# Performance work log

Measured on AMD Instinct MI355X. Metric: run time of the kernel, lower is better.

The kernel has to match this reference:

```python
import jax, jax.numpy as jnp
import numpy as np

N, C, T, H, W = 8, 512, 8, 32, 32
CI = 256          # inter_channels = in_channels // 2
CA = 128          # audio feature dim (hard-coded nn.Linear(128, in_channels))
BN_EPS = 1e-5
LN_EPS = 1e-5


def setup_inputs() -> dict:
    key = jax.random.key(0)
    ks = jax.random.split(key, 8)
    s = 0.02
    f32 = jnp.float32
    return {
        "x": jax.random.normal(ks[0], (N, C, T, H, W), f32),
        "audio": jax.random.normal(ks[1], (N, T, CA), f32),
        "align_W": jax.random.normal(ks[2], (C, CA), f32) * s,
        "align_b": jnp.zeros((C,), f32),
        "Wg": jax.random.normal(ks[3], (CI, C), f32) * s,
        "bg": jnp.zeros((CI,), f32),
        "Wth": jax.random.normal(ks[4], (CI, C), f32) * s,
        "bth": jnp.zeros((CI,), f32),
        "Wph": jax.random.normal(ks[5], (CI, C), f32) * s,
        "bph": jnp.zeros((CI,), f32),
        "Wz": jax.random.normal(ks[6], (C, CI), f32) * s,
        "bz": jnp.zeros((C,), f32),
        "bn_gamma": jnp.ones((C,), f32),
        "bn_beta": jnp.zeros((C,), f32),
        "ln_gamma": jnp.ones((C,), f32),
        "ln_beta": jnp.zeros((C,), f32),
    }


def reference(x, audio, align_W, align_b, Wg, bg, Wth, bth, Wph, bph,
              Wz, bz, bn_gamma, bn_beta, ln_gamma, ln_beta):
    n, c, t, h, w = x.shape
    thw = t * h * w

    # align_channel: Linear(128, C) + ReLU on audio (N,T,128) -> (N,T,C)
    audio_temp = jax.nn.relu(jnp.einsum('ntk,ck->ntc', audio, align_W) + align_b)
    a = audio_temp.transpose(0, 2, 1)  # (N,C,T); broadcast over (H,W) kept implicit

    # 1x1x1 conv projections (== per-token linear maps)
    g_x = (jnp.einsum('oc,ncthw->nthwo', Wg, x) + bg).reshape(n, thw, CI)      # (N,THW,CI)
    theta_x = (jnp.einsum('oc,ncthw->nthwo', Wth, x) + bth).reshape(n, thw, CI)
    phi_a = jnp.einsum('oc,nct->not', Wph, a) + bph[None, :, None]             # (N,CI,T)

    # mode='dot' attention. phi(audio) is constant over (h,w): the full score
    # matrix f[n,s,(t,h,w)] equals f_small[n,s,t], so f@g factorizes exactly.
    f_small = jnp.einsum('nsi,nit->nst', theta_x, phi_a)   # (N,THW,T)
    f_div = f_small / thw                                  # f / N_tokens
    G = g_x.reshape(n, t, h * w, CI).sum(axis=2)           # (N,T,CI): sum of g over repeated hw
    y = jnp.einsum('nst,nto->nso', f_div, G)               # (N,THW,CI)
    y = y.transpose(0, 2, 1).reshape(n, CI, t, h, w)

    # W_z: 1x1x1 conv (CI->C) + BatchNorm3d (training-mode batch stats)
    W_y = jnp.einsum('oc,ncthw->nothw', Wz, y) + bz[None, :, None, None, None]
    mu = W_y.mean(axis=(0, 2, 3, 4), keepdims=True)
    var = W_y.var(axis=(0, 2, 3, 4), keepdims=True)
    W_y = (W_y - mu) * jax.lax.rsqrt(var + BN_EPS)
    W_y = W_y * bn_gamma[None, :, None, None, None] + bn_beta[None, :, None, None, None]

    # residual blend + LayerNorm over channel dim
    z = 0.5 * W_y + 0.5 * x
    zp = z.transpose(0, 2, 3, 4, 1)  # (N,T,H,W,C)
    mu2 = zp.mean(axis=-1, keepdims=True)
    var2 = zp.var(axis=-1, keepdims=True)
    zp = (zp - mu2) * jax.lax.rsqrt(var2 + LN_EPS) * ln_gamma + ln_beta
    z = zp.transpose(0, 4, 1, 2, 3)  # (N,C,T,H,W)
    return z, audio_temp
```

## Files before the change

kernel.cpp:

```cpp
#include <hip/hip_runtime.h>


__global__ __launch_bounds__(256) void k_small1(
    const float* __restrict__ audio, const float* __restrict__ alignW, const float* __restrict__ alignB,
    const float* __restrict__ Wph, const float* __restrict__ bph,
    const float* __restrict__ Wth, const float* __restrict__ bth,
    float* __restrict__ outA, float* __restrict__ constT, float* __restrict__ M)
{
    int b = blockIdx.x; int n = b >> 3; int t = b & 7; int tid = threadIdx.x;
    __shared__ float al[128];
    __shared__ float atl[512];
    __shared__ float phil[256];
    __shared__ float red[256];
    if (tid < 128) al[tid] = audio[(n * 8 + t) * 128 + tid];
    __syncthreads();
    for (int c = tid; c < 512; c += 256) {
        float a0 = alignB[c], a1 = 0.f, a2 = 0.f, a3 = 0.f;
        const float* Wr = alignW + c * 128;
        #pragma unroll 4
        for (int k = 0; k < 128; k += 4) {
            a0 += al[k] * Wr[k];         a1 += al[k + 1] * Wr[k + 1];
            a2 += al[k + 2] * Wr[k + 2]; a3 += al[k + 3] * Wr[k + 3];
        }
        float acc = fmaxf((a0 + a1) + (a2 + a3), 0.f);
        atl[c] = acc;
        outA[(n * 8 + t) * 512 + c] = acc;
    }
    __syncthreads();
    {
        int i = tid;
        float a0 = bph[i], a1 = 0.f, a2 = 0.f, a3 = 0.f;
        const float* Wr = Wph + i * 512;
        #pragma unroll 4
        for (int c = 0; c < 512; c += 4) {
            a0 += Wr[c] * atl[c];         a1 += Wr[c + 1] * atl[c + 1];
            a2 += Wr[c + 2] * atl[c + 2]; a3 += Wr[c + 3] * atl[c + 3];
        }
        float acc = (a0 + a1) + (a2 + a3);
        phil[i] = acc;
        red[i] = acc * bth[i];
    }
    __syncthreads();
    for (int sr = 128; sr > 0; sr >>= 1) {
        if (tid < sr) red[tid] += red[tid + sr];
        __syncthreads();
    }
    if (tid == 0) constT[n * 8 + t] = red[0];
    for (int c = tid; c < 512; c += 256) {
        float a0 = 0.f, a1 = 0.f, a2 = 0.f, a3 = 0.f;
        #pragma unroll 4
        for (int i = 0; i < 256; i += 4) {
            a0 += Wth[i * 512 + c] * phil[i];
            a1 += Wth[(i + 1) * 512 + c] * phil[i + 1];
            a2 += Wth[(i + 2) * 512 + c] * phil[i + 2];
            a3 += Wth[(i + 3) * 512 + c] * phil[i + 3];
        }
        M[n * 4096 + c * 8 + t] = (a0 + a1) + (a2 + a3);
    }
}

__global__ __launch_bounds__(256) void k_xsum(const float* __restrict__ x, float* __restrict__ xs)
{
    int row = blockIdx.x * 4 + (threadIdx.x >> 6);
    int lane = threadIdx.x & 63;
    const float4* p = reinterpret_cast<const float4*>(x + (size_t)row * 1024);
    float s = 0.f;
    #pragma unroll
    for (int k = 0; k < 4; ++k) {
        float4 v = p[lane + 64 * k];
        s += v.x + v.y + v.z + v.w;
    }
    for (int off = 32; off > 0; off >>= 1) s += __shfl_down(s, off);
    if (lane == 0) xs[row] = s;
}

__global__ __launch_bounds__(512, 4) void k_fsmall(
    const float* __restrict__ x, const float* __restrict__ M,
    const float* __restrict__ constT, float* __restrict__ fs,
    float* __restrict__ Part)
{
    int b = blockIdx.x; int n = b >> 6; int s0 = (b & 63) << 7;
    int tid = threadIdx.x; int lane = tid & 63; int wv = tid >> 6;
    __shared__ float Ml[512][8];
    {
        const float4* src = reinterpret_cast<const float4*>(M + n * 4096);
        float4* dst = reinterpret_cast<float4*>(&Ml[0][0]);
        for (int i = tid; i < 1024; i += 512) dst[i] = src[i];
    }
    __syncthreads();
    const float* xb = x + (size_t)n * 4194304 + s0 + lane * 2;
    float2 p2[8];
    #pragma unroll
    for (int k = 0; k < 8; ++k) p2[k] = make_float2(0.f, 0.f);
    #pragma unroll 8
    for (int j = 0; j < 64; ++j) {
        int c = wv * 64 + j;
        float2 xv = *reinterpret_cast<const float2*>(xb + (size_t)c * 8192);
        float4 m0 = *reinterpret_cast<const float4*>(&Ml[c][0]);
        float4 m1 = *reinterpret_cast<const float4*>(&Ml[c][4]);
        p2[0].x = fmaf(xv.x, m0.x, p2[0].x); p2[0].y = fmaf(xv.y, m0.x, p2[0].y);
        p2[1].x = fmaf(xv.x, m0.y, p2[1].x); p2[1].y = fmaf(xv.y, m0.y, p2[1].y);
        p2[2].x = fmaf(xv.x, m0.z, p2[2].x); p2[2].y = fmaf(xv.y, m0.z, p2[2].y);
        p2[3].x = fmaf(xv.x, m0.w, p2[3].x); p2[3].y = fmaf(xv.y, m0.w, p2[3].y);
        p2[4].x = fmaf(xv.x, m1.x, p2[4].x); p2[4].y = fmaf(xv.y, m1.x, p2[4].y);
        p2[5].x = fmaf(xv.x, m1.y, p2[5].x); p2[5].y = fmaf(xv.y, m1.y, p2[5].y);
        p2[6].x = fmaf(xv.x, m1.z, p2[6].x); p2[6].y = fmaf(xv.y, m1.z, p2[6].y);
        p2[7].x = fmaf(xv.x, m1.w, p2[7].x); p2[7].y = fmaf(xv.y, m1.w, p2[7].y);
    }
    __shared__ float ldsT[8][8][130];
    #pragma unroll
    for (int k = 0; k < 8; ++k)
        *reinterpret_cast<float2*>(&ldsT[wv][k][lane * 2]) = p2[k];
    __syncthreads();
    __shared__ float partm[2][44];
    if (tid < 128) {
        int tok = tid; int wq = tid >> 6;
        const float* ct = constT + n * 8;
        float q[8];
        #pragma unroll
        for (int k = 0; k < 8; ++k) {
            float v = ct[k];
            #pragma unroll
            for (int g = 0; g < 8; ++g) v += ldsT[g][k][tok];
            q[k] = v;
        }
        float4* op = reinterpret_cast<float4*>(fs + ((size_t)n * 8192 + s0 + tok) * 8);
        op[0] = make_float4(q[0], q[1], q[2], q[3]);
        op[1] = make_float4(q[4], q[5], q[6], q[7]);
        float mom[44];
        {
            int idx = 8;
            for (int t1 = 0; t1 < 8; ++t1) {
                mom[t1] = q[t1];
                for (int t2 = t1; t2 < 8; ++t2) { mom[idx] = q[t1] * q[t2]; ++idx; }
            }
        }
        for (int k = 0; k < 44; ++k)
            for (int off = 32; off > 0; off >>= 1) mom[k] += __shfl_down(mom[k], off);
        if ((tid & 63) == 0)
            for (int k = 0; k < 44; ++k) partm[wq][k] = mom[k];
    }
    __syncthreads();
    if (tid < 44) Part[b * 44 + tid] = partm[0][tid] + partm[1][tid];
}

__global__ __launch_bounds__(256) void k_small2(
    const float* __restrict__ xs, const float* __restrict__ Wg, const float* __restrict__ bg,
    const float* __restrict__ Wz, float* __restrict__ GW)
{
    int b = blockIdx.x; int n = b >> 3; int t = b & 7; int tid = threadIdx.x;
    __shared__ float xsl[512];
    __shared__ float gl[256];
    for (int c = tid; c < 512; c += 256) xsl[c] = xs[(n * 512 + c) * 8 + t];
    __syncthreads();
    {
        int o = tid;
        float a0 = 1024.f * bg[o], a1 = 0.f, a2 = 0.f, a3 = 0.f;
        const float* Wr = Wg + o * 512;
        #pragma unroll 4
        for (int c = 0; c < 512; c += 4) {
            a0 += Wr[c] * xsl[c];         a1 += Wr[c + 1] * xsl[c + 1];
            a2 += Wr[c + 2] * xsl[c + 2]; a3 += Wr[c + 3] * xsl[c + 3];
        }
        gl[o] = (a0 + a1) + (a2 + a3);
    }
    __syncthreads();
    for (int c = tid; c < 512; c += 256) {
        float a0 = 0.f, a1 = 0.f, a2 = 0.f, a3 = 0.f;
        const float* Wr = Wz + c * 256;
        #pragma unroll 4
        for (int o = 0; o < 256; o += 4) {
            a0 += Wr[o] * gl[o];         a1 += Wr[o + 1] * gl[o + 1];
            a2 += Wr[o + 2] * gl[o + 2]; a3 += Wr[o + 3] * gl[o + 3];
        }
        GW[(n * 8 + t) * 512 + c] = (a0 + a1) + (a2 + a3);
    }
}

__global__ __launch_bounds__(512) void k_bn(
    const float* __restrict__ Part, const float* __restrict__ GW,
    const float* __restrict__ bz, const float* __restrict__ bng, const float* __restrict__ bnb,
    const float* __restrict__ lng, const float* __restrict__ lnb,
    float* __restrict__ pack0, float* __restrict__ gw2)
{
    int n0 = blockIdx.x; int c = threadIdx.x;
    __shared__ float Fl[64];
    __shared__ float S2l[512];
    if (c < 352) {
        int n = c / 44, k = c % 44;
        float v = 0.f;
        for (int i = 0; i < 64; ++i) v += Part[(n * 64 + i) * 44 + k];
        if (k < 8) Fl[n * 8 + k] = v;
        else {
            int kk = k - 8; int t1 = 0;
            while (kk >= 8 - t1) { kk -= 8 - t1; ++t1; }
            int t2 = t1 + kk;
            S2l[n * 64 + t1 * 8 + t2] = v;
            S2l[n * 64 + t2 * 8 + t1] = v;
        }
    }
    __syncthreads();
    const float r = 1.f / 8192.f;
    float meanu = 0.f, e2 = 0.f;
    for (int n = 0; n < 8; ++n) {
        float g[8];
        for (int t = 0; t < 8; ++t) g[t] = GW[(n * 8 + t) * 512 + c];
        for (int t = 0; t < 8; ++t) meanu += Fl[n * 8 + t] * g[t];
        for (int t1 = 0; t1 < 8; ++t1)
            for (int t2 = 0; t2 < 8; ++t2) e2 += S2l[n * 64 + t1 * 8 + t2] * g[t1] * g[t2];
    }
    const float invCnt = 1.f / 65536.f;
    meanu *= r * invCnt;
    e2 *= r * r * invCnt;
    float var = fmaxf(e2 - meanu * meanu, 0.f);
    float bzv = bz[c];
    float mean = meanu + bzv;
    float sc = bng[c] * rsqrtf(var + 1e-5f);
    float sh = bnb[c] - mean * sc;
    if (n0 == 0) {
        float4 pk;
        pk.x = 0.5f * (bzv * sc + sh);
        pk.y = lng[c];
        pk.z = lnb[c];
        pk.w = 0.f;
        *reinterpret_cast<float4*>(pack0 + c * 4) = pk;
    }
    float scale = 0.5f * r * sc;
    for (int t = 0; t < 8; ++t)
        gw2[((size_t)n0 * 512 + c) * 8 + t] = GW[(n0 * 8 + t) * 512 + c] * scale;
}

__global__ __launch_bounds__(512, 4) void k_final(
    const float* __restrict__ x, const float* __restrict__ fs,
    const float* __restrict__ pack0, const float* __restrict__ gw2,
    float* __restrict__ outZ)
{
    int b = blockIdx.x; int n = b >> 6; int s0 = (b & 63) << 7;
    int tid = threadIdx.x; int lane = tid & 63; int wv = tid >> 6;
    __shared__ float GWl[512][8];
    __shared__ float4 PKl[512];
    __shared__ float redS[2][8][130];
    {
        const float4* src = reinterpret_cast<const float4*>(gw2 + (size_t)n * 4096);
        float4* dst = reinterpret_cast<float4*>(&GWl[0][0]);
        for (int i = tid; i < 1024; i += 512) dst[i] = src[i];
        const float4* ps = reinterpret_cast<const float4*>(pack0);
        PKl[tid] = ps[tid];
    }
    __syncthreads();
    float4 fA0, fB0, fA1, fB1;
    {
        const float4* fp = reinterpret_cast<const float4*>(fs + ((size_t)n * 8192 + s0 + lane * 2) * 8);
        fA0 = fp[0]; fB0 = fp[1]; fA1 = fp[2]; fB1 = fp[3];
    }
    const size_t xbase = (size_t)n * 4194304 + s0 + lane * 2;
    float2 s1 = make_float2(0.f, 0.f), sq = make_float2(0.f, 0.f);
    #pragma unroll 8
    for (int j = 0; j < 64; ++j) {
        int c = wv * 64 + j;
        float2 xv = *reinterpret_cast<const float2*>(&x[xbase + (size_t)c * 8192]);
        float4 g0 = *reinterpret_cast<const float4*>(&GWl[c][0]);
        float4 g1 = *reinterpret_cast<const float4*>(&GWl[c][4]);
        float pk0 = PKl[c].x;
        float z0 = pk0 + 0.5f * xv.x
            + fA0.x * g0.x + fA0.y * g0.y + fA0.z * g0.z + fA0.w * g0.w
            + fB0.x * g1.x + fB0.y * g1.y + fB0.z * g1.z + fB0.w * g1.w;
        float z1 = pk0 + 0.5f * xv.y
            + fA1.x * g0.x + fA1.y * g0.y + fA1.z * g0.z + fA1.w * g0.w
            + fB1.x * g1.x + fB1.y * g1.y + fB1.z * g1.z + fB1.w * g1.w;
        s1.x += z0; sq.x += z0 * z0;
        s1.y += z1; sq.y += z1 * z1;
    }
    *reinterpret_cast<float2*>(&redS[0][wv][lane * 2]) = s1;
    *reinterpret_cast<float2*>(&redS[1][wv][lane * 2]) = sq;
    __syncthreads();
    float mean0, rstd0, mean1, rstd1;
    {
        int t0 = lane * 2, t1 = lane * 2 + 1;
        float a0 = 0.f, q0 = 0.f, a1 = 0.f, q1 = 0.f;
        #pragma unroll
        for (int g = 0; g < 8; ++g) {
            a0 += redS[0][g][t0]; q0 += redS[1][g][t0];
            a1 += redS[0][g][t1]; q1 += redS[1][g][t1];
        }
        mean0 = a0 * (1.f / 512.f);
        rstd0 = rsqrtf(fmaxf(q0 * (1.f / 512.f) - mean0 * mean0, 0.f) + 1e-5f);
        mean1 = a1 * (1.f / 512.f);
        rstd1 = rsqrtf(fmaxf(q1 * (1.f / 512.f) - mean1 * mean1, 0.f) + 1e-5f);
    }
    #pragma unroll 8
    for (int j = 0; j < 64; ++j) {
        int c = wv * 64 + j;
        float2 xv = *reinterpret_cast<const float2*>(&x[xbase + (size_t)c * 8192]);
        float4 g0 = *reinterpret_cast<const float4*>(&GWl[c][0]);
        float4 g1 = *reinterpret_cast<const float4*>(&GWl[c][4]);
        float4 pk = PKl[c];
        float z0 = pk.x + 0.5f * xv.x
            + fA0.x * g0.x + fA0.y * g0.y + fA0.z * g0.z + fA0.w * g0.w
            + fB0.x * g1.x + fB0.y * g1.y + fB0.z * g1.z + fB0.w * g1.w;
        float z1 = pk.x + 0.5f * xv.y
            + fA1.x * g0.x + fA1.y * g0.y + fA1.z * g0.z + fA1.w * g0.w
            + fB1.x * g1.x + fB1.y * g1.y + fB1.z * g1.z + fB1.w * g1.w;
        float2 o;
        o.x = (z0 - mean0) * rstd0 * pk.y + pk.z;
        o.y = (z1 - mean1) * rstd1 * pk.y + pk.z;
        *reinterpret_cast<float2*>(&outZ[xbase + (size_t)c * 8192]) = o;
    }
}

extern "C" void kernel_launch(void* const* d_in, const int* in_sizes, int n_in,
                              void* d_out, int out_size, void* d_ws, size_t ws_size,
                              hipStream_t stream)
{
    const float* x      = (const float*)d_in[0];
    const float* audio  = (const float*)d_in[1];
    const float* alignW = (const float*)d_in[2];
    const float* alignB = (const float*)d_in[3];
    const float* Wg     = (const float*)d_in[4];
    const float* bg     = (const float*)d_in[5];
    const float* Wth    = (const float*)d_in[6];
    const float* bth    = (const float*)d_in[7];
    const float* Wph    = (const float*)d_in[8];
    const float* bph    = (const float*)d_in[9];
    const float* Wz     = (const float*)d_in[10];
    const float* bz     = (const float*)d_in[11];
    const float* bng    = (const float*)d_in[12];
    const float* bnb    = (const float*)d_in[13];
    const float* lng    = (const float*)d_in[14];
    const float* lnb    = (const float*)d_in[15];
    float* outZ = (float*)d_out;
    float* outA = outZ + 33554432;

    uintptr_t pa = ((uintptr_t)d_ws + 255) & ~(uintptr_t)255;
    float* w = (float*)pa;

    float* constT = w;
    float* M      = w + 64;
    float* XS     = w + 32832;
    float* GW     = w + 65600;
    float* Part   = w + 98368;
    float* pack0  = w + 120896;
    float* gw2    = w + 122944;
    float* fsm    = w + 155712;

    k_xsum<<<8192, 256, 0, stream>>>(x, XS);
    k_small1<<<64, 256, 0, stream>>>(audio, alignW, alignB, Wph, bph, Wth, bth, outA, constT, M);
    k_fsmall<<<512, 512, 0, stream>>>(x, M, constT, fsm, Part);
    k_small2<<<64, 256, 0, stream>>>(XS, Wg, bg, Wz, GW);
    k_bn<<<8, 512, 0, stream>>>(Part, GW, bz, bng, bnb, lng, lnb, pack0, gw2);
    k_final<<<512, 512, 0, stream>>>(x, fsm, pack0, gw2, outZ);
}
```

Before: 197.5 us.

## Fuse small precompute kernels and fold BN stats into final kernel

Merges k_small1 and k_small2 into a single k_pre launch, and removes k_bn. Each k_final block now recomputes the BatchNorm statistics from the partial moments and builds its own scaled GW tile, which cuts the launch count from six to four. It also raises the unroll factor on the channel loops and switches output writes to nontemporal stores. In exchange, every one of the 512 final blocks repeats the reduction over Part and the GW statistics, which adds redundant work and global reads at the start of each block.

```diff
diff --git a/kernel.cpp b/kernel.cpp
--- a/kernel.cpp
+++ b/kernel.cpp
@@ -1,63 +1,7 @@
 #include <hip/hip_runtime.h>
 
 
-__global__ __launch_bounds__(256) void k_small1(
-    const float* __restrict__ audio, const float* __restrict__ alignW, const float* __restrict__ alignB,
-    const float* __restrict__ Wph, const float* __restrict__ bph,
-    const float* __restrict__ Wth, const float* __restrict__ bth,
-    float* __restrict__ outA, float* __restrict__ constT, float* __restrict__ M)
-{
-    int b = blockIdx.x; int n = b >> 3; int t = b & 7; int tid = threadIdx.x;
-    __shared__ float al[128];
-    __shared__ float atl[512];
-    __shared__ float phil[256];
-    __shared__ float red[256];
-    if (tid < 128) al[tid] = audio[(n * 8 + t) * 128 + tid];
-    __syncthreads();
-    for (int c = tid; c < 512; c += 256) {
-        float a0 = alignB[c], a1 = 0.f, a2 = 0.f, a3 = 0.f;
-        const float* Wr = alignW + c * 128;
-        #pragma unroll 4
-        for (int k = 0; k < 128; k += 4) {
-            a0 += al[k] * Wr[k];         a1 += al[k + 1] * Wr[k + 1];
-            a2 += al[k + 2] * Wr[k + 2]; a3 += al[k + 3] * Wr[k + 3];
-        }
-        float acc = fmaxf((a0 + a1) + (a2 + a3), 0.f);
-        atl[c] = acc;
-        outA[(n * 8 + t) * 512 + c] = acc;
-    }
-    __syncthreads();
-    {
-        int i = tid;
-        float a0 = bph[i], a1 = 0.f, a2 = 0.f, a3 = 0.f;
-        const float* Wr = Wph + i * 512;
-        #pragma unroll 4
-        for (int c = 0; c < 512; c += 4) {
-            a0 += Wr[c] * atl[c];         a1 += Wr[c + 1] * atl[c + 1];
-            a2 += Wr[c + 2] * atl[c + 2]; a3 += Wr[c + 3] * atl[c + 3];
-        }
-        float acc = (a0 + a1) + (a2 + a3);
-        phil[i] = acc;
-        red[i] = acc * bth[i];
-    }
-    __syncthreads();
-    for (int sr = 128; sr > 0; sr >>= 1) {
-        if (tid < sr) red[tid] += red[tid + sr];
-        __syncthreads();
-    }
-    if (tid == 0) constT[n * 8 + t] = red[0];
-    for (int c = tid; c < 512; c += 256) {
-        float a0 = 0.f, a1 = 0.f, a2 = 0.f, a3 = 0.f;
-        #pragma unroll 4
-        for (int i = 0; i < 256; i += 4) {
-            a0 += Wth[i * 512 + c] * phil[i];
-            a1 += Wth[(i + 1) * 512 + c] * phil[i + 1];
-            a2 += Wth[(i + 2) * 512 + c] * phil[i + 2];
-            a3 += Wth[(i + 3) * 512 + c] * phil[i + 3];
-        }
-        M[n * 4096 + c * 8 + t] = (a0 + a1) + (a2 + a3);
-    }
-}
+typedef float __attribute__((ext_vector_type(2))) f32x2;
 
 __global__ __launch_bounds__(256) void k_xsum(const float* __restrict__ x, float* __restrict__ xs)
 {
@@ -74,6 +18,93 @@
     if (lane == 0) xs[row] = s;
 }
 
+__global__ __launch_bounds__(256) void k_pre(
+    const float* __restrict__ audio, const float* __restrict__ alignW, const float* __restrict__ alignB,
+    const float* __restrict__ Wph, const float* __restrict__ bph,
+    const float* __restrict__ Wth, const float* __restrict__ bth,
+    const float* __restrict__ xs, const float* __restrict__ Wg, const float* __restrict__ bg,
+    const float* __restrict__ Wz,
+    float* __restrict__ outA, float* __restrict__ constT, float* __restrict__ M,
+    float* __restrict__ GW)
+{
+    int b = blockIdx.x; int n = b >> 3; int t = b & 7; int tid = threadIdx.x;
+    __shared__ float al[128];
+    __shared__ float atl[512];
+    __shared__ float phil[256];
+    __shared__ float red[256];
+    __shared__ float xsl[512];
+    __shared__ float gl[256];
+    if (tid < 128) al[tid] = audio[(n * 8 + t) * 128 + tid];
+    __syncthreads();
+    for (int c = tid; c < 512; c += 256) {
+        float a0 = alignB[c], a1 = 0.f, a2 = 0.f, a3 = 0.f;
+        const float* Wr = alignW + c * 128;
+        #pragma unroll 4
+        for (int k = 0; k < 128; k += 4) {
+            a0 += al[k] * Wr[k];         a1 += al[k + 1] * Wr[k + 1];
+            a2 += al[k + 2] * Wr[k + 2]; a3 += al[k + 3] * Wr[k + 3];
+        }
+        float acc = fmaxf((a0 + a1) + (a2 + a3), 0.f);
+        atl[c] = acc;
+        outA[(n * 8 + t) * 512 + c] = acc;
+    }
+    __syncthreads();
+    {
+        int i = tid;
+        float a0 = bph[i], a1 = 0.f, a2 = 0.f, a3 = 0.f;
+        const float* Wr = Wph + i * 512;
+        #pragma unroll 4
+        for (int c = 0; c < 512; c += 4) {
+            a0 += Wr[c] * atl[c];         a1 += Wr[c + 1] * atl[c + 1];
+            a2 += Wr[c + 2] * atl[c + 2]; a3 += Wr[c + 3] * atl[c + 3];
+        }
+        float acc = (a0 + a1) + (a2 + a3);
+        phil[i] = acc;
+        red[i] = acc * bth[i];
+    }
+    __syncthreads();
+    for (int sr = 128; sr > 0; sr >>= 1) {
+        if (tid < sr) red[tid] += red[tid + sr];
+        __syncthreads();
+    }
+    if (tid == 0) constT[n * 8 + t] = red[0];
+    for (int c = tid; c < 512; c += 256) {
+        float a0 = 0.f, a1 = 0.f, a2 = 0.f, a3 = 0.f;
+        #pragma unroll 4
+        for (int i = 0; i < 256; i += 4) {
+            a0 += Wth[i * 512 + c] * phil[i];
+            a1 += Wth[(i + 1) * 512 + c] * phil[i + 1];
+            a2 += Wth[(i + 2) * 512 + c] * phil[i + 2];
+            a3 += Wth[(i + 3) * 512 + c] * phil[i + 3];
+        }
+        M[n * 4096 + c * 8 + t] = (a0 + a1) + (a2 + a3);
+    }
+    for (int c = tid; c < 512; c += 256) xsl[c] = xs[(n * 512 + c) * 8 + t];
+    __syncthreads();
+    {
+        int o = tid;
+        float a0 = 1024.f * bg[o], a1 = 0.f, a2 = 0.f, a3 = 0.f;
+        const float* Wr = Wg + o * 512;
+        #pragma unroll 4
+        for (int c = 0; c < 512; c += 4) {
+            a0 += Wr[c] * xsl[c];         a1 += Wr[c + 1] * xsl[c + 1];
+            a2 += Wr[c + 2] * xsl[c + 2]; a3 += Wr[c + 3] * xsl[c + 3];
+        }
+        gl[o] = (a0 + a1) + (a2 + a3);
+    }
+    __syncthreads();
+    for (int c = tid; c < 512; c += 256) {
+        float a0 = 0.f, a1 = 0.f, a2 = 0.f, a3 = 0.f;
+        const float* Wr = Wz + c * 256;
+        #pragma unroll 4
+        for (int o = 0; o < 256; o += 4) {
+            a0 += Wr[o] * gl[o];         a1 += Wr[o + 1] * gl[o + 1];
+            a2 += Wr[o + 2] * gl[o + 2]; a3 += Wr[o + 3] * gl[o + 3];
+        }
+        GW[(n * 8 + t) * 512 + c] = (a0 + a1) + (a2 + a3);
+    }
+}
+
 __global__ __launch_bounds__(512, 4) void k_fsmall(
     const float* __restrict__ x, const float* __restrict__ M,
     const float* __restrict__ constT, float* __restrict__ fs,
@@ -92,7 +123,7 @@
     float2 p2[8];
     #pragma unroll
     for (int k = 0; k < 8; ++k) p2[k] = make_float2(0.f, 0.f);
-    #pragma unroll 8
+    #pragma unroll 16
     for (int j = 0; j < 64; ++j) {
         int c = wv * 64 + j;
         float2 xv = *reinterpret_cast<const float2*>(xb + (size_t)c * 8192);
@@ -144,108 +175,69 @@
     if (tid < 44) Part[b * 44 + tid] = partm[0][tid] + partm[1][tid];
 }
 
-__global__ __launch_bounds__(256) void k_small2(
-    const float* __restrict__ xs, const float* __restrict__ Wg, const float* __restrict__ bg,
-    const float* __restrict__ Wz, float* __restrict__ GW)
-{
-    int b = blockIdx.x; int n = b >> 3; int t = b & 7; int tid = threadIdx.x;
-    __shared__ float xsl[512];
-    __shared__ float gl[256];
-    for (int c = tid; c < 512; c += 256) xsl[c] = xs[(n * 512 + c) * 8 + t];
-    __syncthreads();
-    {
-        int o = tid;
-        float a0 = 1024.f * bg[o], a1 = 0.f, a2 = 0.f, a3 = 0.f;
-        const float* Wr = Wg + o * 512;
-        #pragma unroll 4
-        for (int c = 0; c < 512; c += 4) {
-            a0 += Wr[c] * xsl[c];         a1 += Wr[c + 1] * xsl[c + 1];
-            a2 += Wr[c + 2] * xsl[c + 2]; a3 += Wr[c + 3] * xsl[c + 3];
-        }
-        gl[o] = (a0 + a1) + (a2 + a3);
-    }
-    __syncthreads();
-    for (int c = tid; c < 512; c += 256) {
-        float a0 = 0.f, a1 = 0.f, a2 = 0.f, a3 = 0.f;
-        const float* Wr = Wz + c * 256;
-        #pragma unroll 4
-        for (int o = 0; o < 256; o += 4) {
-            a0 += Wr[o] * gl[o];         a1 += Wr[o + 1] * gl[o + 1];
-            a2 += Wr[o + 2] * gl[o + 2]; a3 += Wr[o + 3] * gl[o + 3];
-        }
-        GW[(n * 8 + t) * 512 + c] = (a0 + a1) + (a2 + a3);
-    }
-}
-
-__global__ __launch_bounds__(512) void k_bn(
+__global__ __launch_bounds__(512, 4) void k_final(
+    const float* __restrict__ x, const float* __restrict__ fs,
     const float* __restrict__ Part, const float* __restrict__ GW,
     const float* __restrict__ bz, const float* __restrict__ bng, const float* __restrict__ bnb,
     const float* __restrict__ lng, const float* __restrict__ lnb,
-    float* __restrict__ pack0, float* __restrict__ gw2)
-{
-    int n0 = blockIdx.x; int c = threadIdx.x;
+    float* __restrict__ outZ)
+{
+    int b = blockIdx.x; int n = b >> 6; int s0 = (b & 63) << 7;
+    int tid = threadIdx.x; int lane = tid & 63; int wv = tid >> 6;
+    __shared__ float GWl[512][8];
+    __shared__ float4 PKl[512];
+    __shared__ float redS[2][8][130];
     __shared__ float Fl[64];
     __shared__ float S2l[512];
-    if (c < 352) {
-        int n = c / 44, k = c % 44;
+    if (tid < 352) {
+        int n2 = tid / 44, k = tid % 44;
         float v = 0.f;
-        for (int i = 0; i < 64; ++i) v += Part[(n * 64 + i) * 44 + k];
-        if (k < 8) Fl[n * 8 + k] = v;
+        for (int i = 0; i < 64; ++i) v += Part[(n2 * 64 + i) * 44 + k];
+        if (k < 8) Fl[n2 * 8 + k] = v;
         else {
             int kk = k - 8; int t1 = 0;
             while (kk >= 8 - t1) { kk -= 8 - t1; ++t1; }
             int t2 = t1 + kk;
-            S2l[n * 64 + t1 * 8 + t2] = v;
-            S2l[n * 64 + t2 * 8 + t1] = v;
-        }
-    }
-    __syncthreads();
-    const float r = 1.f / 8192.f;
-    float meanu = 0.f, e2 = 0.f;
-    for (int n = 0; n < 8; ++n) {
-        float g[8];
-        for (int t = 0; t < 8; ++t) g[t] = GW[(n * 8 + t) * 512 + c];
-        for (int t = 0; t < 8; ++t) meanu += Fl[n * 8 + t] * g[t];
-        for (int t1 = 0; t1 < 8; ++t1)
-            for (int t2 = 0; t2 < 8; ++t2) e2 += S2l[n * 64 + t1 * 8 + t2] * g[t1] * g[t2];
-    }
-    const float invCnt = 1.f / 65536.f;
-    meanu *= r * invCnt;
-    e2 *= r * r * invCnt;
-    float var = fmaxf(e2 - meanu * meanu, 0.f);
-    float bzv = bz[c];
-    float mean = meanu + bzv;
-    float sc = bng[c] * rsqrtf(var + 1e-5f);
-    float sh = bnb[c] - mean * sc;
-    if (n0 == 0) {
+            S2l[n2 * 64 + t1 * 8 + t2] = v;
+            S2l[n2 * 64 + t2 * 8 + t1] = v;
+        }
+    }
+    __syncthreads();
+    {
+        int c = tid;
+        const float r = 1.f / 8192.f;
+        float meanu = 0.f, e2 = 0.f;
+        float gmine[8];
+        for (int n2 = 0; n2 < 8; ++n2) {
+            float g[8];
+            #pragma unroll
+            for (int t = 0; t < 8; ++t) g[t] = GW[(n2 * 8 + t) * 512 + c];
+            if (n2 == n) {
+                #pragma unroll
+                for (int t = 0; t < 8; ++t) gmine[t] = g[t];
+            }
+            #pragma unroll
+            for (int t = 0; t < 8; ++t) meanu += Fl[n2 * 8 + t] * g[t];
+            for (int t1 = 0; t1 < 8; ++t1)
+                #pragma unroll
+                for (int t2 = 0; t2 < 8; ++t2) e2 += S2l[n2 * 64 + t1 * 8 + t2] * g[t1] * g[t2];
+        }
+        const float invCnt = 1.f / 65536.f;
+        meanu *= r * invCnt;
+        e2 *= r * r * invCnt;
+        float var = fmaxf(e2 - meanu * meanu, 0.f);
+        float bzv = bz[c];
+        float sc = bng[c] * rsqrtf(var + 1e-5f);
+        float sh = bnb[c] - (meanu + bzv) * sc;
         float4 pk;
         pk.x = 0.5f * (bzv * sc + sh);
         pk.y = lng[c];
         pk.z = lnb[c];
         pk.w = 0.f;
-        *reinterpret_cast<float4*>(pack0 + c * 4) = pk;
-    }
-    float scale = 0.5f * r * sc;
-    for (int t = 0; t < 8; ++t)
-        gw2[((size_t)n0 * 512 + c) * 8 + t] = GW[(n0 * 8 + t) * 512 + c] * scale;
-}
-
-__global__ __launch_bounds__(512, 4) void k_final(
-    const float* __restrict__ x, const float* __restrict__ fs,
-    const float* __restrict__ pack0, const float* __restrict__ gw2,
-    float* __restrict__ outZ)
-{
-    int b = blockIdx.x; int n = b >> 6; int s0 = (b & 63) << 7;
-    int tid = threadIdx.x; int lane = tid & 63; int wv = tid >> 6;
-    __shared__ float GWl[512][8];
-    __shared__ float4 PKl[512];
-    __shared__ float redS[2][8][130];
-    {
-        const float4* src = reinterpret_cast<const float4*>(gw2 + (size_t)n * 4096);
-        float4* dst = reinterpret_cast<float4*>(&GWl[0][0]);
-        for (int i = tid; i < 1024; i += 512) dst[i] = src[i];
-        const float4* ps = reinterpret_cast<const float4*>(pack0);
-        PKl[tid] = ps[tid];
+        PKl[c] = pk;
+        float scale = 0.5f * r * sc;
+        #pragma unroll
+        for (int t = 0; t < 8; ++t) GWl[c][t] = gmine[t] * scale;
     }
     __syncthreads();
     float4 fA0, fB0, fA1, fB1;
@@ -255,7 +247,7 @@
     }
     const size_t xbase = (size_t)n * 4194304 + s0 + lane * 2;
     float2 s1 = make_float2(0.f, 0.f), sq = make_float2(0.f, 0.f);
-    #pragma unroll 8
+    #pragma unroll 16
     for (int j = 0; j < 64; ++j) {
         int c = wv * 64 + j;
         float2 xv = *reinterpret_cast<const float2*>(&x[xbase + (size_t)c * 8192]);
@@ -288,7 +280,7 @@
         mean1 = a1 * (1.f / 512.f);
         rstd1 = rsqrtf(fmaxf(q1 * (1.f / 512.f) - mean1 * mean1, 0.f) + 1e-5f);
     }
-    #pragma unroll 8
+    #pragma unroll 16
     for (int j = 0; j < 64; ++j) {
         int c = wv * 64 + j;
         float2 xv = *reinterpret_cast<const float2*>(&x[xbase + (size_t)c * 8192]);
@@ -301,10 +293,10 @@
         float z1 = pk.x + 0.5f * xv.y
             + fA1.x * g0.x + fA1.y * g0.y + fA1.z * g0.z + fA1.w * g0.w
             + fB1.x * g1.x + fB1.y * g1.y + fB1.z * g1.z + fB1.w * g1.w;
-        float2 o;
+        f32x2 o;
         o.x = (z0 - mean0) * rstd0 * pk.y + pk.z;
         o.y = (z1 - mean1) * rstd1 * pk.y + pk.z;
-        *reinterpret_cast<float2*>(&outZ[xbase + (size_t)c * 8192]) = o;
+        __builtin_nontemporal_store(o, reinterpret_cast<f32x2*>(&outZ[xbase + (size_t)c * 8192]));
     }
 }
 
@@ -339,14 +331,11 @@
     float* XS     = w + 32832;
     float* GW     = w + 65600;
     float* Part   = w + 98368;
-    float* pack0  = w + 120896;
-    float* gw2    = w + 122944;
-    float* fsm    = w + 155712;
+    float* fsm    = w + 120896;
 
     k_xsum<<<8192, 256, 0, stream>>>(x, XS);
-    k_small1<<<64, 256, 0, stream>>>(audio, alignW, alignB, Wph, bph, Wth, bth, outA, constT, M);
+    k_pre<<<64, 256, 0, stream>>>(audio, alignW, alignB, Wph, bph, Wth, bth,
+                                  XS, Wg, bg, Wz, outA, constT, M, GW);
     k_fsmall<<<512, 512, 0, stream>>>(x, M, constT, fsm, Part);
-    k_small2<<<64, 256, 0, stream>>>(XS, Wg, bg, Wz, GW);
-    k_bn<<<8, 512, 0, stream>>>(Part, GW, bz, bng, bnb, lng, lnb, pack0, gw2);
-    k_final<<<512, 512, 0, stream>>>(x, fsm, pack0, gw2, outZ);
-}
+    k_final<<<512, 512, 0, stream>>>(x, fsm, Part, GW, bz, bng, bnb, lng, lnb, outZ);
+}
```

Measured after the change: 181.4 us. -8.1%, faster.
